# Kernel tuning notes

Hardware: AMD Instinct MI355X
Metric: run time of the kernel (lower is better)

## Reference

```python
import jax, jax.numpy as jnp
import numpy as np


def _lstm_scan(x_seq, W, U, b):
    # x_seq: [T, in_dim]; Keras gate order i, f, g(c), o; sigmoid/tanh activations.
    units = W.shape[1] // 4
    xz = x_seq @ W + b  # [T, 4*units], precompute input contribution

    def step(carry, xz_t):
        h, c = carry
        z = xz_t + h @ U
        i, f, g, o = jnp.split(z, 4)
        i = jax.nn.sigmoid(i)
        f = jax.nn.sigmoid(f)
        g = jnp.tanh(g)
        o = jax.nn.sigmoid(o)
        c_new = f * c + i * g
        h_new = o * jnp.tanh(c_new)
        return (h_new, c_new), h_new

    h0 = jnp.zeros((units,), dtype=x_seq.dtype)
    c0 = jnp.zeros((units,), dtype=x_seq.dtype)
    (_, _), hs = jax.lax.scan(step, (h0, c0), xz)
    return hs  # [T, units]


def setup_inputs() -> dict:
    key = jax.random.key(0)
    ks = jax.random.split(key, 6)
    var_num, g_dim, d, vocab = 256, 1024, 512, 32000
    s = lambda fi, fo: (2.0 / (fi + fo)) ** 0.5
    return {
        "context": jax.random.normal(ks[0], (var_num, g_dim), jnp.float32),
        "Wm": jax.random.normal(ks[1], (g_dim, d), jnp.float32) * s(g_dim, d),
        "bm": jnp.zeros((d,), jnp.float32),
        "W": jax.random.normal(ks[2], (d, 4 * d), jnp.float32) * s(d, 4 * d),
        "U": jax.random.normal(ks[3], (d, 4 * d), jnp.float32) * s(d, 4 * d),
        "b": jnp.zeros((4 * d,), jnp.float32),
        "Wl": jax.random.normal(ks[4], (d, vocab), jnp.float32) * s(d, vocab),
        "bl": jnp.zeros((vocab,), jnp.float32),
        "max_subtoken_len": 8,
    }


def reference(context, Wm, bm, W, U, b, Wl, bl, max_subtoken_len):
    # Dense merge of func/graph embedding (cat_func_g_emb branch)
    merged = context @ Wm + bm  # [var_num, d]
    var_num = merged.shape[0]
    # Original loop feeds the SAME [1, var_num, d] sequence through the LSTM
    # max_subtoken_len times, carrying (h, c) across iterations => one long
    # scan over the tiled sequence of length S * var_num.
    x_seq = jnp.tile(merged, (max_subtoken_len, 1))  # [S*var_num, d]
    hs = _lstm_scan(x_seq, W, U, b)  # [S*var_num, units]
    hs = hs.reshape(max_subtoken_len, var_num, -1)  # [S, var_num, units]
    logits = jnp.einsum("svd,dk->svk", hs, Wl) + bl  # [S, var_num, vocab]
    return jnp.transpose(logits, (1, 0, 2))  # [var_num, S, vocab]
```

## Files before the change

kernel.cpp:

```cpp
#include <hip/hip_runtime.h>
#include <stdint.h>

#define D 512
#define T 2048
#define VOCAB 32000
#define NWG 16

typedef __attribute__((ext_vector_type(8))) short short8;
typedef __attribute__((ext_vector_type(4))) float f32x4;
typedef __attribute__((ext_vector_type(8))) unsigned short u16x8;
typedef __attribute__((ext_vector_type(2))) __fp16 f16x2;

__device__ __forceinline__ float fast_rcp(float x) { return __builtin_amdgcn_rcpf(x); }
__device__ __forceinline__ float sigm(float x) { return fast_rcp(1.0f + __expf(-x)); }
__device__ __forceinline__ float tanh_fast(float x) {
  float e = __expf(2.0f * x);
  return 1.0f - 2.0f * fast_rcp(e + 1.0f);
}
__device__ __forceinline__ unsigned short f2bf(float f) {
  unsigned u = __float_as_uint(f);
  unsigned r = u + 0x7fffu + ((u >> 16) & 1u);
  return (unsigned short)(r >> 16);
}
__device__ __forceinline__ uint64_t AL(const uint64_t* p) {
  return __hip_atomic_load(p, __ATOMIC_RELAXED, __HIP_MEMORY_SCOPE_AGENT);
}
union U32H2 { unsigned u; f16x2 h; };

__global__ __launch_bounds__(512) void prep_kernel(
    const float* __restrict__ ctx, const float* __restrict__ Wm,
    const float* __restrict__ bm, const float* __restrict__ W,
    const float* __restrict__ b, float* __restrict__ xz)
{
  __shared__ float ctx_s[4][1024];
  __shared__ float mg_s[4][512];
  const int tid = threadIdx.x;
  const int r0 = blockIdx.x * 4;

  for (int i = tid; i < 1024; i += 512) {
    int rr = i >> 8, c4 = (i & 255) * 4;
    *(float4*)&ctx_s[rr][c4] = *(const float4*)&ctx[(size_t)(r0 + rr) * 1024 + c4];
  }
  __syncthreads();
  {
    const int rr = tid >> 7, cg = (tid & 127) * 4;
    float a0 = bm[cg], a1 = bm[cg + 1], a2 = bm[cg + 2], a3 = bm[cg + 3];
    for (int k = 0; k < 1024; k += 4) {
      float4 cv = *(float4*)&ctx_s[rr][k];
      #pragma unroll
      for (int kk = 0; kk < 4; kk++) {
        float cc = (kk == 0) ? cv.x : (kk == 1) ? cv.y : (kk == 2) ? cv.z : cv.w;
        float4 wv = *(const float4*)&Wm[(size_t)(k + kk) * 512 + cg];
        a0 += cc * wv.x; a1 += cc * wv.y; a2 += cc * wv.z; a3 += cc * wv.w;
      }
    }
    *(float4*)&mg_s[rr][cg] = make_float4(a0, a1, a2, a3);
  }
  __syncthreads();
  {
    const int rr = tid >> 7, cg = (tid & 127) * 16;
    float acc[16];
    #pragma unroll
    for (int c = 0; c < 16; c++) acc[c] = b[cg + c];
    for (int k = 0; k < 512; k += 4) {
      float4 mv = *(float4*)&mg_s[rr][k];
      #pragma unroll
      for (int kk = 0; kk < 4; kk++) {
        float cc = (kk == 0) ? mv.x : (kk == 1) ? mv.y : (kk == 2) ? mv.z : mv.w;
        #pragma unroll
        for (int c4 = 0; c4 < 4; c4++) {
          float4 wv = *(const float4*)&W[(size_t)(k + kk) * 2048 + cg + c4 * 4];
          acc[c4 * 4 + 0] += cc * wv.x; acc[c4 * 4 + 1] += cc * wv.y;
          acc[c4 * 4 + 2] += cc * wv.z; acc[c4 * 4 + 3] += cc * wv.w;
        }
      }
    }
    #pragma unroll
    for (int c4 = 0; c4 < 4; c4++)
      *(float4*)&xz[(size_t)(r0 + rr) * 2048 + cg + c4 * 4] =
          make_float4(acc[c4 * 4], acc[c4 * 4 + 1], acc[c4 * 4 + 2], acc[c4 * 4 + 3]);
  }
}

__global__ __launch_bounds__(256) void wl_convert_kernel(
    const float* __restrict__ Wl, unsigned short* __restrict__ Wlt)
{
  const int c = blockIdx.x * 256 + threadIdx.x;
  for (int k8 = 0; k8 < 64; k8++) {
    u16x8 v;
    #pragma unroll
    for (int e = 0; e < 8; e++)
      v[e] = f2bf(Wl[(size_t)(k8 * 8 + e) * VOCAB + c]);
    *(u16x8*)&Wlt[(size_t)c * 512 + k8 * 8] = v;
  }
}

__global__ __launch_bounds__(256) void uconv_kernel(
    const float* __restrict__ U, unsigned* __restrict__ Up)
{
  const int p = blockIdx.x;
  const int c0 = threadIdx.x * 8;
  const int r_lo = (p >> 5) * 64 + (p & 31);
  const float* lo = &U[(size_t)r_lo * 2048 + c0];
  const float* hi = &U[(size_t)(r_lo + 32) * 2048 + c0];
  unsigned outv[8];
  #pragma unroll
  for (int c = 0; c < 8; c++) {
    U32H2 w;
    w.h[0] = (__fp16)lo[c];
    w.h[1] = (__fp16)hi[c];
    outv[c] = w.u;
  }
  #pragma unroll
  for (int c4 = 0; c4 < 2; c4++)
    *(uint4*)&Up[(size_t)p * 2048 + c0 + c4 * 4] =
        make_uint4(outv[c4 * 4], outv[c4 * 4 + 1], outv[c4 * 4 + 2], outv[c4 * 4 + 3]);
}

__global__
__attribute__((amdgpu_flat_work_group_size(512, 512)))
__attribute__((amdgpu_waves_per_eu(2, 2)))
void lstm_kernel(
    const float* __restrict__ xz, const unsigned* __restrict__ Up,
    uint64_t* __restrict__ hb, unsigned short* __restrict__ hs)
{
  __shared__ float h_lds[512];
  __shared__ float z_lds[128];
  const int tid = threadIdx.x;
  const int wg = blockIdx.x;
  const int rb = tid & 31;
  const int cb = tid >> 5;
  const int gate = cb >> 2;
  const int gcol0 = gate * 512 + wg * 32 + (cb & 3) * 8;

  uint4 uv[16];
  #pragma unroll
  for (int ep = 0; ep < 8; ep++) {
    const unsigned* ap = &Up[(size_t)(ep * 32 + rb) * 2048 + gcol0];
    asm volatile("global_load_dwordx4 %0, %1, off"
                 : "=v"(uv[ep * 2]) : "v"(ap));
    asm volatile("global_load_dwordx4 %0, %1, off offset:16"
                 : "=v"(uv[ep * 2 + 1]) : "v"(ap));
  }
  asm volatile("s_waitcnt vmcnt(0)" ::: "memory");
  unsigned u2[8][8];
  #pragma unroll
  for (int ep = 0; ep < 8; ep++) {
    uint4 a = uv[ep * 2], b4 = uv[ep * 2 + 1];
    u2[ep][0] = a.x; u2[ep][1] = a.y; u2[ep][2] = a.z; u2[ep][3] = a.w;
    u2[ep][4] = b4.x; u2[ep][5] = b4.y; u2[ep][6] = b4.z; u2[ep][7] = b4.w;
  }

  float creg = 0.0f;

  for (int t = 0; t < T; t++) {
    #pragma unroll
    for (int ep = 0; ep < 8; ep++) {
      #pragma unroll
      for (int c = 0; c < 8; c++) asm volatile("" : "+v"(u2[ep][c]));
    }
    float xzv0, xzv1, xzv2, xzv3;
    if (tid < 32) {
      const float* xp = &xz[(size_t)(t & 255) * 2048 + wg * 32 + tid];
      xzv0 = xp[0]; xzv1 = xp[512]; xzv2 = xp[1024]; xzv3 = xp[1536];
    }
    {
      const uint64_t* hw = hb + (size_t)((t & 1) << 9) + tid;
      uint64_t wv;
      for (;;) {
        wv = AL(hw);
        if ((unsigned)(wv >> 32) == (unsigned)t) break;
      }
      h_lds[tid] = __uint_as_float((unsigned)wv);
    }
    __syncthreads();

    float zp[8];
    #pragma unroll
    for (int c = 0; c < 8; c++) zp[c] = 0.0f;
    #pragma unroll
    for (int ep = 0; ep < 8; ep++) {
      float hlo = h_lds[rb + 64 * ep];
      float hhi = h_lds[rb + 64 * ep + 32];
      f16x2 h2 = __builtin_amdgcn_cvt_pkrtz(hlo, hhi);
      #pragma unroll
      for (int c = 0; c < 8; c++) {
        U32H2 w; w.u = u2[ep][c];
        zp[c] = __builtin_amdgcn_fdot2(h2, w.h, zp[c], false);
      }
    }
    #pragma unroll
    for (int m = 1; m < 32; m <<= 1) {
      #pragma unroll
      for (int c = 0; c < 8; c++) zp[c] += __shfl_xor(zp[c], m, 64);
    }
    if (rb == 0) {
      *(float4*)&z_lds[cb * 8]     = make_float4(zp[0], zp[1], zp[2], zp[3]);
      *(float4*)&z_lds[cb * 8 + 4] = make_float4(zp[4], zp[5], zp[6], zp[7]);
    }
    __syncthreads();
    if (tid < 32) {
      float zi = z_lds[tid]       + xzv0;
      float zf = z_lds[32 + tid]  + xzv1;
      float zg = z_lds[64 + tid]  + xzv2;
      float zo = z_lds[96 + tid]  + xzv3;
      float ig = sigm(zi), fg = sigm(zf), gg = tanh_fast(zg), og = sigm(zo);
      creg = fg * creg + ig * gg;
      float h = og * tanh_fast(creg);
      uint64_t pk = ((uint64_t)(unsigned)(t + 1) << 32) | (uint64_t)__float_as_uint(h);
      __hip_atomic_store(&hb[(size_t)(((t + 1) & 1) << 9) + wg * 32 + tid], pk,
                         __ATOMIC_RELAXED, __HIP_MEMORY_SCOPE_AGENT);
      hs[(size_t)t * 512 + wg * 32 + tid] = f2bf(h);
    }
  }
}

__global__ __launch_bounds__(256) void logits_kernel(
    const unsigned short* __restrict__ hs, const unsigned short* __restrict__ Wlt,
    const float* __restrict__ bl, float* __restrict__ out)
{
  __shared__ unsigned short As[128][40];
  __shared__ unsigned short Bs[128][40];
  const int tid = threadIdx.x;
  const int bx = blockIdx.x, by = blockIdx.y;
  const int lane = tid & 63, w = tid >> 6;
  const int wr = w >> 1, wc = w & 1;

  f32x4 acc[4][4];
  #pragma unroll
  for (int i = 0; i < 4; i++) {
    #pragma unroll
    for (int j = 0; j < 4; j++) acc[i][j] = (f32x4){0.0f, 0.0f, 0.0f, 0.0f};
  }

  for (int kk = 0; kk < 512; kk += 32) {
    #pragma unroll
    for (int i = 0; i < 2; i++) {
      int chunk = tid * 2 + i;
      int r = chunk >> 2, c8 = (chunk & 3) * 8;
      *(uint4*)&As[r][c8] = *(const uint4*)&hs[(size_t)(by * 128 + r) * 512 + kk + c8];
      *(uint4*)&Bs[r][c8] = *(const uint4*)&Wlt[(size_t)(bx * 128 + r) * 512 + kk + c8];
    }
    __syncthreads();
    short8 af[4], bf[4];
    #pragma unroll
    for (int fr = 0; fr < 4; fr++)
      af[fr] = *(const short8*)&As[wr * 64 + fr * 16 + (lane & 15)][(lane >> 4) * 8];
    #pragma unroll
    for (int fc = 0; fc < 4; fc++)
      bf[fc] = *(const short8*)&Bs[wc * 64 + fc * 16 + (lane & 15)][(lane >> 4) * 8];
    #pragma unroll
    for (int fr = 0; fr < 4; fr++) {
      #pragma unroll
      for (int fc = 0; fc < 4; fc++)
        acc[fr][fc] = __builtin_amdgcn_mfma_f32_16x16x32_bf16(af[fr], bf[fc], acc[fr][fc], 0, 0, 0);
    }
    __syncthreads();
  }

  #pragma unroll
  for (int fc = 0; fc < 4; fc++) {
    int col = bx * 128 + wc * 64 + fc * 16 + (lane & 15);
    float blv = bl[col];
    #pragma unroll
    for (int fr = 0; fr < 4; fr++) {
      int row0 = by * 128 + wr * 64 + fr * 16 + (lane >> 4) * 4;
      #pragma unroll
      for (int j = 0; j < 4; j++) {
        int row = row0 + j;
        int orow = (row & 255) * 8 + (row >> 8);
        out[(size_t)orow * VOCAB + col] = acc[fr][fc][j] + blv;
      }
    }
  }
}

extern "C" void kernel_launch(void* const* d_in, const int* in_sizes, int n_in,
                              void* d_out, int out_size, void* d_ws, size_t ws_size,
                              hipStream_t stream)
{
  const float* ctx = (const float*)d_in[0];
  const float* Wm  = (const float*)d_in[1];
  const float* bm  = (const float*)d_in[2];
  const float* W   = (const float*)d_in[3];
  const float* U   = (const float*)d_in[4];
  const float* b   = (const float*)d_in[5];
  const float* Wl  = (const float*)d_in[6];
  const float* bl  = (const float*)d_in[7];
  float* out = (float*)d_out;

  char* ws = (char*)d_ws;
  uint64_t* hb        = (uint64_t*)ws;
  float* xz           = (float*)(ws + 65536);
  unsigned short* hs  = (unsigned short*)(ws + 65536 + (1 << 21));
  unsigned* Up        = (unsigned*)(ws + 65536 + (2 << 21));
  unsigned short* Wlt = (unsigned short*)(ws + 65536 + (3 << 21));

  hipMemsetAsync(hb, 0, 8192, stream);
  prep_kernel<<<dim3(64), dim3(512), 0, stream>>>(ctx, Wm, bm, W, b, xz);
  uconv_kernel<<<dim3(256), dim3(256), 0, stream>>>(U, Up);
  wl_convert_kernel<<<dim3(125), dim3(256), 0, stream>>>(Wl, Wlt);

  void* args[] = { (void*)&xz, (void*)&Up, (void*)&hb, (void*)&hs };
  hipLaunchCooperativeKernel((void*)lstm_kernel, dim3(NWG), dim3(512), args, 0, stream);

  logits_kernel<<<dim3(250, 16), dim3(256), 0, stream>>>(hs, Wlt, bl, out);
}
```

Before: 4.980 ms.

## Restructure LSTM step to drop second barrier via transpose-reduce and local h

The U weights are re-laid out so each thread holds all four gates for two hidden units. The per-column butterfly reduction becomes a transpose-style reduction that leaves gate sums distributed across lanes, which removes the z_lds round trip and the second __syncthreads per timestep. Polling is reduced to 120 threads, each reading four h values, and skips the workgroup's own slice, which is written straight into a double-buffered LDS h array. This shortens the serial per-step critical path of the recurrence, at the cost of more complex lane indexing and reliance on LDS double-buffering for correctness.

Result: faster. 4.784 ms (-3.9%).

```diff
diff --git a/kernel.cpp b/kernel.cpp
--- a/kernel.cpp
+++ b/kernel.cpp
@@ -95,52 +95,51 @@
   }
 }
 
-__global__ __launch_bounds__(256) void uconv_kernel(
-    const float* __restrict__ U, unsigned* __restrict__ Up)
-{
-  const int p = blockIdx.x;
-  const int c0 = threadIdx.x * 8;
-  const int r_lo = (p >> 5) * 64 + (p & 31);
-  const float* lo = &U[(size_t)r_lo * 2048 + c0];
-  const float* hi = &U[(size_t)(r_lo + 32) * 2048 + c0];
+__global__ __launch_bounds__(256) void uconv2_kernel(
+    const float* __restrict__ U, unsigned* __restrict__ Upr)
+{
+  const int blk = blockIdx.x;
+  const int wg = blk >> 4, cb = blk & 15;
+  const int rb = threadIdx.x & 31, ep = threadIdx.x >> 5;
+  const int u0 = wg * 32 + cb * 2;
+  const int r = rb + 64 * ep;
   unsigned outv[8];
   #pragma unroll
-  for (int c = 0; c < 8; c++) {
-    U32H2 w;
-    w.h[0] = (__fp16)lo[c];
-    w.h[1] = (__fp16)hi[c];
-    outv[c] = w.u;
-  }
-  #pragma unroll
-  for (int c4 = 0; c4 < 2; c4++)
-    *(uint4*)&Up[(size_t)p * 2048 + c0 + c4 * 4] =
-        make_uint4(outv[c4 * 4], outv[c4 * 4 + 1], outv[c4 * 4 + 2], outv[c4 * 4 + 3]);
+  for (int g = 0; g < 4; g++) {
+    float2 lo = *(const float2*)&U[(size_t)r * 2048 + g * 512 + u0];
+    float2 hi = *(const float2*)&U[(size_t)(r + 32) * 2048 + g * 512 + u0];
+    U32H2 w0; w0.h[0] = (__fp16)lo.x; w0.h[1] = (__fp16)hi.x;
+    U32H2 w1; w1.h[0] = (__fp16)lo.y; w1.h[1] = (__fp16)hi.y;
+    outv[g * 2] = w0.u; outv[g * 2 + 1] = w1.u;
+  }
+  unsigned* dst = Upr + ((size_t)(wg * 512 + cb * 32 + rb)) * 64 + ep * 8;
+  *(uint4*)dst = make_uint4(outv[0], outv[1], outv[2], outv[3]);
+  *(uint4*)(dst + 4) = make_uint4(outv[4], outv[5], outv[6], outv[7]);
 }
 
 __global__
 __attribute__((amdgpu_flat_work_group_size(512, 512)))
 __attribute__((amdgpu_waves_per_eu(2, 2)))
 void lstm_kernel(
-    const float* __restrict__ xz, const unsigned* __restrict__ Up,
+    const float* __restrict__ xz, const unsigned* __restrict__ Upr,
     uint64_t* __restrict__ hb, unsigned short* __restrict__ hs)
 {
-  __shared__ float h_lds[512];
-  __shared__ float z_lds[128];
+  __shared__ float h_lds[2][512];
   const int tid = threadIdx.x;
   const int wg = blockIdx.x;
   const int rb = tid & 31;
+  const int lane = tid & 63;
   const int cb = tid >> 5;
-  const int gate = cb >> 2;
-  const int gcol0 = gate * 512 + wg * 32 + (cb & 3) * 8;
-
+  const int u0 = wg * 32 + cb * 2;
+  const bool gl = (rb < 2);
+  const bool mypoll = (tid < 128) && ((tid >> 3) != wg);
+
+  const unsigned* ubase = Upr + ((size_t)(wg * 512 + tid)) * 64;
   uint4 uv[16];
   #pragma unroll
-  for (int ep = 0; ep < 8; ep++) {
-    const unsigned* ap = &Up[(size_t)(ep * 32 + rb) * 2048 + gcol0];
-    asm volatile("global_load_dwordx4 %0, %1, off"
-                 : "=v"(uv[ep * 2]) : "v"(ap));
-    asm volatile("global_load_dwordx4 %0, %1, off offset:16"
-                 : "=v"(uv[ep * 2 + 1]) : "v"(ap));
+  for (int i = 0; i < 16; i++) {
+    const unsigned* ap = ubase + i * 4;
+    asm volatile("global_load_dwordx4 %0, %1, off" : "=v"(uv[i]) : "v"(ap));
   }
   asm volatile("s_waitcnt vmcnt(0)" ::: "memory");
   unsigned u2[8][8];
@@ -151,7 +150,9 @@
     u2[ep][4] = b4.x; u2[ep][5] = b4.y; u2[ep][6] = b4.z; u2[ep][7] = b4.w;
   }
 
+  h_lds[0][tid] = 0.0f;
   float creg = 0.0f;
+  const int b0 = rb & 1, b1 = (rb >> 1) & 1, b2v = (rb >> 2) & 1;
 
   for (int t = 0; t < T; t++) {
     #pragma unroll
@@ -159,19 +160,26 @@
       #pragma unroll
       for (int c = 0; c < 8; c++) asm volatile("" : "+v"(u2[ep][c]));
     }
-    float xzv0, xzv1, xzv2, xzv3;
-    if (tid < 32) {
-      const float* xp = &xz[(size_t)(t & 255) * 2048 + wg * 32 + tid];
-      xzv0 = xp[0]; xzv1 = xp[512]; xzv2 = xp[1024]; xzv3 = xp[1536];
-    }
-    {
-      const uint64_t* hw = hb + (size_t)((t & 1) << 9) + tid;
-      uint64_t wv;
+    float xv0, xv1, xv2, xv3;
+    if (gl) {
+      const float* xp = &xz[(size_t)(t & 255) * 2048 + u0 + rb];
+      xv0 = xp[0]; xv1 = xp[512]; xv2 = xp[1024]; xv3 = xp[1536];
+    }
+    const int par = t & 1;
+    if (mypoll) {
+      uint64_t* hw = hb + ((size_t)par << 9) + tid * 4;
+      const unsigned tt = (unsigned)t;
       for (;;) {
-        wv = AL(hw);
-        if ((unsigned)(wv >> 32) == (unsigned)t) break;
-      }
-      h_lds[tid] = __uint_as_float((unsigned)wv);
+        uint64_t w0 = AL(hw), w1 = AL(hw + 1), w2 = AL(hw + 2), w3 = AL(hw + 3);
+        if (((unsigned)(w0 >> 32) == tt) & ((unsigned)(w1 >> 32) == tt) &
+            ((unsigned)(w2 >> 32) == tt) & ((unsigned)(w3 >> 32) == tt)) {
+          h_lds[par][tid * 4 + 0] = __uint_as_float((unsigned)w0);
+          h_lds[par][tid * 4 + 1] = __uint_as_float((unsigned)w1);
+          h_lds[par][tid * 4 + 2] = __uint_as_float((unsigned)w2);
+          h_lds[par][tid * 4 + 3] = __uint_as_float((unsigned)w3);
+          break;
+        }
+      }
     }
     __syncthreads();
 
@@ -180,8 +188,8 @@
     for (int c = 0; c < 8; c++) zp[c] = 0.0f;
     #pragma unroll
     for (int ep = 0; ep < 8; ep++) {
-      float hlo = h_lds[rb + 64 * ep];
-      float hhi = h_lds[rb + 64 * ep + 32];
+      float hlo = h_lds[par][rb + 64 * ep];
+      float hhi = h_lds[par][rb + 64 * ep + 32];
       f16x2 h2 = __builtin_amdgcn_cvt_pkrtz(hlo, hhi);
       #pragma unroll
       for (int c = 0; c < 8; c++) {
@@ -189,28 +197,44 @@
         zp[c] = __builtin_amdgcn_fdot2(h2, w.h, zp[c], false);
       }
     }
-    #pragma unroll
-    for (int m = 1; m < 32; m <<= 1) {
-      #pragma unroll
-      for (int c = 0; c < 8; c++) zp[c] += __shfl_xor(zp[c], m, 64);
-    }
-    if (rb == 0) {
-      *(float4*)&z_lds[cb * 8]     = make_float4(zp[0], zp[1], zp[2], zp[3]);
-      *(float4*)&z_lds[cb * 8 + 4] = make_float4(zp[4], zp[5], zp[6], zp[7]);
-    }
-    __syncthreads();
-    if (tid < 32) {
-      float zi = z_lds[tid]       + xzv0;
-      float zf = z_lds[32 + tid]  + xzv1;
-      float zg = z_lds[64 + tid]  + xzv2;
-      float zo = z_lds[96 + tid]  + xzv3;
-      float ig = sigm(zi), fg = sigm(zf), gg = tanh_fast(zg), og = sigm(zo);
+    float q[4];
+    #pragma unroll
+    for (int j = 0; j < 4; j++) {
+      float send = b0 ? zp[2 * j] : zp[2 * j + 1];
+      float recv = __shfl_xor(send, 1, 64);
+      q[j] = (b0 ? zp[2 * j + 1] : zp[2 * j]) + recv;
+    }
+    float r2[2];
+    #pragma unroll
+    for (int j = 0; j < 2; j++) {
+      float send = b1 ? q[2 * j] : q[2 * j + 1];
+      float recv = __shfl_xor(send, 2, 64);
+      r2[j] = (b1 ? q[2 * j + 1] : q[2 * j]) + recv;
+    }
+    float z;
+    {
+      float send = b2v ? r2[0] : r2[1];
+      float recv = __shfl_xor(send, 4, 64);
+      z = (b2v ? r2[1] : r2[0]) + recv;
+    }
+    z += __shfl_xor(z, 8, 64);
+    z += __shfl_xor(z, 16, 64);
+    float zf = __shfl(z, (lane & 32) + 2 + b0, 64);
+    float zg = __shfl(z, (lane & 32) + 4 + b0, 64);
+    float zo = __shfl(z, (lane & 32) + 6 + b0, 64);
+
+    if (gl) {
+      float ig = sigm(z + xv0);
+      float fg = sigm(zf + xv1);
+      float gg = tanh_fast(zg + xv2);
+      float og = sigm(zo + xv3);
       creg = fg * creg + ig * gg;
       float h = og * tanh_fast(creg);
       uint64_t pk = ((uint64_t)(unsigned)(t + 1) << 32) | (uint64_t)__float_as_uint(h);
-      __hip_atomic_store(&hb[(size_t)(((t + 1) & 1) << 9) + wg * 32 + tid], pk,
+      __hip_atomic_store(&hb[((size_t)((t + 1) & 1) << 9) + u0 + rb], pk,
                          __ATOMIC_RELAXED, __HIP_MEMORY_SCOPE_AGENT);
-      hs[(size_t)t * 512 + wg * 32 + tid] = f2bf(h);
+      h_lds[(t + 1) & 1][u0 + rb] = h;
+      hs[(size_t)t * 512 + u0 + rb] = f2bf(h);
     }
   }
 }
@@ -293,15 +317,15 @@
   uint64_t* hb        = (uint64_t*)ws;
   float* xz           = (float*)(ws + 65536);
   unsigned short* hs  = (unsigned short*)(ws + 65536 + (1 << 21));
-  unsigned* Up        = (unsigned*)(ws + 65536 + (2 << 21));
+  unsigned* Upr       = (unsigned*)(ws + 65536 + (2 << 21));
   unsigned short* Wlt = (unsigned short*)(ws + 65536 + (3 << 21));
 
   hipMemsetAsync(hb, 0, 8192, stream);
   prep_kernel<<<dim3(64), dim3(512), 0, stream>>>(ctx, Wm, bm, W, b, xz);
-  uconv_kernel<<<dim3(256), dim3(256), 0, stream>>>(U, Up);
+  uconv2_kernel<<<dim3(256), dim3(256), 0, stream>>>(U, Upr);
   wl_convert_kernel<<<dim3(125), dim3(256), 0, stream>>>(Wl, Wlt);
 
-  void* args[] = { (void*)&xz, (void*)&Up, (void*)&hb, (void*)&hs };
+  void* args[] = { (void*)&xz, (void*)&Upr, (void*)&hb, (void*)&hs };
   hipLaunchCooperativeKernel((void*)lstm_kernel, dim3(NWG), dim3(512), args, 0, stream);
 
   logits_kernel<<<dim3(250, 16), dim3(256), 0, stream>>>(hs, Wlt, bl, out);
```
